# Kernel tuning notes

Measured on AMD Instinct MI355X. Metric: run time of the kernel, lower is better.

The kernel has to match this reference:

```python
import jax, jax.numpy as jnp
import numpy as np

D_MODEL, D_K, D_V, N_HEADS = 1024, 64, 64, 16
BS, N_CTX = 2, 2048


def setup_inputs() -> dict:
    key = jax.random.key(0)
    ks = jax.random.split(key, 8)
    s = 0.02
    return {
        "x": jax.random.normal(ks[0], (BS, N_CTX, D_MODEL), dtype=jnp.float32),
        "Wq": jax.random.normal(ks[1], (D_K * N_HEADS, D_MODEL), dtype=jnp.float32) * s,
        "bq": jnp.zeros((D_K * N_HEADS,), dtype=jnp.float32),
        "Wk": jax.random.normal(ks[2], (D_K * N_HEADS, D_MODEL), dtype=jnp.float32) * s,
        "bk": jnp.zeros((D_K * N_HEADS,), dtype=jnp.float32),
        "Wv": jax.random.normal(ks[3], (D_V * N_HEADS, D_MODEL), dtype=jnp.float32) * s,
        "bv": jnp.zeros((D_V * N_HEADS,), dtype=jnp.float32),
        "Wo": jax.random.normal(ks[4], (D_MODEL, D_V * N_HEADS), dtype=jnp.float32) * s,
    }


def reference(x, Wq, bq, Wk, bk, Wv, bv, Wo):
    bs, n_ctx, d_model = x.shape
    # projections (torch Linear: y = x @ W.T + b)
    q = x @ Wq.T + bq  # (bs, n, H*dk)
    k = x @ Wk.T + bk
    v = x @ Wv.T + bv
    split = lambda t, d: t.reshape(bs, n_ctx, N_HEADS, d).transpose(0, 2, 1, 3)
    Q, K, V = split(q, D_K), split(k, D_K), split(v, D_V)  # (bs, H, n, d)
    scores = jnp.einsum('bhqd,bhkd->bhqk', Q / jnp.sqrt(jnp.float32(D_K)), K)
    # causal mask: x + (1 - 1/tril(ones)) == 0 on/below diag, -inf above
    causal = jnp.tril(jnp.ones((n_ctx, n_ctx), dtype=bool))
    scores = jnp.where(causal, scores, -jnp.inf)
    attn = jax.nn.softmax(scores, axis=-1)
    out = jnp.einsum('bhqk,bhkd->bhqd', attn, V)  # (bs, H, n, dv)
    out = out.transpose(0, 2, 1, 3).reshape(bs, n_ctx, N_HEADS * D_V)
    return out @ Wo.T  # no bias on output projection
```

## Files before the change

kernel.cpp:

```cpp
#include <hip/hip_runtime.h>
#include <hip/hip_bf16.h>


using bf16x8   = __attribute__((ext_vector_type(8))) __bf16;
using f32x4    = __attribute__((ext_vector_type(4))) float;
using ushort4v = __attribute__((ext_vector_type(4))) unsigned short;

__device__ __forceinline__ unsigned short f2bf(float f) {
    unsigned int u = __float_as_uint(f);
    u += 0x7FFFu + ((u >> 16) & 1u);
    return (unsigned short)(u >> 16);
}

__device__ __forceinline__ unsigned cvtpk(float lo, float hi) {
    unsigned r;
    asm("v_cvt_pk_bf16_f32 %0, %1, %2" : "=v"(r) : "v"(lo), "v"(hi));
    return r;
}

__device__ __forceinline__ void gll16(const void* g, void* l) {
    __builtin_amdgcn_global_load_lds(
        (const __attribute__((address_space(1))) void*)g,
        (__attribute__((address_space(3))) void*)l, 16, 0, 0);
}

__global__ __launch_bounds__(256) void cast_bf16_kernel(
    const float* __restrict__ in, unsigned short* __restrict__ out, int n4) {
    int i = blockIdx.x * 256 + threadIdx.x;
    if (i >= n4) return;
    float4 f = reinterpret_cast<const float4*>(in)[i];
    ushort4v o;
    o.x = f2bf(f.x); o.y = f2bf(f.y); o.z = f2bf(f.z); o.w = f2bf(f.w);
    reinterpret_cast<ushort4v*>(out)[i] = o;
}

__global__ __launch_bounds__(256) void cast_w4_kernel(
    const float* __restrict__ w0, const float* __restrict__ w1,
    const float* __restrict__ w2, const float* __restrict__ w3,
    unsigned short* __restrict__ o0, unsigned short* __restrict__ o1,
    unsigned short* __restrict__ o2, unsigned short* __restrict__ o3) {
    const int z = blockIdx.y;
    const float* in = (z == 0) ? w0 : (z == 1) ? w1 : (z == 2) ? w2 : w3;
    unsigned short* out = (z == 0) ? o0 : (z == 1) ? o1 : (z == 2) ? o2 : o3;
    int i = blockIdx.x * 256 + threadIdx.x;
    float4 f = reinterpret_cast<const float4*>(in)[i];
    ushort4v o;
    o.x = f2bf(f.x); o.y = f2bf(f.y); o.z = f2bf(f.z); o.w = f2bf(f.w);
    reinterpret_cast<ushort4v*>(out)[i] = o;
}

__device__ __forceinline__ void gemm_core_128x64(
    const unsigned short* __restrict__ A, const unsigned short* __restrict__ B,
    int m0, int n0, int K,
    unsigned short* As, unsigned short* Bs, f32x4 acc[4][2]) {
    const int tid = threadIdx.x;
    const int lane = tid & 63;
    const int wid = tid >> 6;
    const int wr = wid >> 1, wc = wid & 1;
    const int l16 = lane & 15, lg = lane >> 4;

#pragma unroll
    for (int i = 0; i < 4; i++)
#pragma unroll
        for (int j = 0; j < 2; j++) acc[i][j] = f32x4{0.f, 0.f, 0.f, 0.f};

    const int srow = lane >> 2;
    const int scol = (lane & 3) * 8;
    const unsigned short* Ab0 = &A[(size_t)(m0 + wid * 16 + srow) * K + scol];
    const unsigned short* Ab1 = &A[(size_t)(m0 + 64 + wid * 16 + srow) * K + scol];
    const unsigned short* Bb0 = &B[(size_t)(n0 + wid * 16 + srow) * K + scol];
    unsigned short* AsW0 = As + (wid * 16) * 32;
    unsigned short* AsW1 = As + (64 + wid * 16) * 32;
    unsigned short* BsW0 = Bs + (wid * 16) * 32;

    for (int k0 = 0; k0 < K; k0 += 32) {
        __syncthreads();
        gll16(Ab0 + k0, AsW0);
        gll16(Ab1 + k0, AsW1);
        gll16(Bb0 + k0, BsW0);
        __syncthreads();
        bf16x8 af[4], bfr[2];
#pragma unroll
        for (int i = 0; i < 4; i++)
            af[i] = *reinterpret_cast<const bf16x8*>(&As[(64 * wr + 16 * i + l16) * 32 + 8 * lg]);
#pragma unroll
        for (int j = 0; j < 2; j++)
            bfr[j] = *reinterpret_cast<const bf16x8*>(&Bs[(32 * wc + 16 * j + l16) * 32 + 8 * lg]);
#pragma unroll
        for (int i = 0; i < 4; i++)
#pragma unroll
            for (int j = 0; j < 2; j++)
                acc[i][j] = __builtin_amdgcn_mfma_f32_16x16x32_bf16(af[i], bfr[j], acc[i][j], 0, 0, 0);
    }
}

__global__ __launch_bounds__(256) void gemm_qkv_kernel(
    const unsigned short* __restrict__ xbf,
    const unsigned short* __restrict__ wq, const unsigned short* __restrict__ wk,
    const unsigned short* __restrict__ wv,
    const float* __restrict__ bq, const float* __restrict__ bk, const float* __restrict__ bv,
    unsigned short* __restrict__ q_ws, unsigned short* __restrict__ k_ws,
    unsigned short* __restrict__ vt_ws) {
    __shared__ __align__(16) unsigned short As[128 * 32];
    __shared__ __align__(16) unsigned short Bs[64 * 32];
    const int z = blockIdx.z;
    const unsigned short* W = (z == 0) ? wq : ((z == 1) ? wk : wv);
    const float* bias = (z == 0) ? bq : ((z == 1) ? bk : bv);
    const float scale = (z == 0) ? 0.125f * 1.44269504f : 1.0f;
    const int m0 = blockIdx.y * 128;
    const int n0 = blockIdx.x * 64;

    f32x4 acc[4][2];
    gemm_core_128x64(xbf, W, m0, n0, 1024, As, Bs, acc);

    const int tid = threadIdx.x;
    const int lane = tid & 63;
    const int wid = tid >> 6;
    const int wr = wid >> 1, wc = wid & 1;
    const int l16 = lane & 15, lg = lane >> 4;

#pragma unroll
    for (int j = 0; j < 2; j++) {
        const int c = n0 + 32 * wc + 16 * j + l16;
        const float bc = bias[c];
        const int h = c >> 6, d = c & 63;
#pragma unroll
        for (int i = 0; i < 4; i++) {
            const int mb = m0 + 64 * wr + 16 * i + 4 * lg;
            if (z < 2) {
                unsigned short* dst = (z == 0) ? q_ws : k_ws;
#pragma unroll
                for (int r = 0; r < 4; r++) {
                    int m = mb + r;
                    int b = m >> 11, n = m & 2047;
                    float v = (acc[i][j][r] + bc) * scale;
                    dst[(((b * 16 + h) * 2048 + n) << 6) + d] = f2bf(v);
                }
            } else {
                int b = mb >> 11, n = mb & 2047;
                ushort4v pk;
                pk.x = f2bf(acc[i][j][0] + bc);
                pk.y = f2bf(acc[i][j][1] + bc);
                pk.z = f2bf(acc[i][j][2] + bc);
                pk.w = f2bf(acc[i][j][3] + bc);
                *reinterpret_cast<ushort4v*>(&vt_ws[((b * 16 + h) * 64 + d) * 2048 + n]) = pk;
            }
        }
    }
}

__global__ __launch_bounds__(256) void attn_kernel(
    const unsigned short* __restrict__ q_ws, const unsigned short* __restrict__ k_ws,
    const unsigned short* __restrict__ vt_ws, unsigned short* __restrict__ attn_out) {
    __shared__ __align__(16) unsigned short P_lds[4][2][16][40];
    const int tid = threadIdx.x;
    const int wid = tid >> 6, lane = tid & 63;
    const int l16 = lane & 15, lg = lane >> 4;
    const int gwid = blockIdx.x * 4 + wid;
    const int bh = gwid >> 6;
    const int p = gwid & 63;
    const int qA0 = p << 4;
    const int qB0 = 2032 - (p << 4);
    const unsigned short* qb = q_ws + bh * (2048 * 64);
    const unsigned short* kb = k_ws + bh * (2048 * 64);
    const unsigned short* vb = vt_ws + bh * (64 * 2048);

    bf16x8 aqA0 = *reinterpret_cast<const bf16x8*>(&qb[(qA0 + l16) * 64 + 8 * lg]);
    bf16x8 aqA1 = *reinterpret_cast<const bf16x8*>(&qb[(qA0 + l16) * 64 + 32 + 8 * lg]);
    bf16x8 aqB0 = *reinterpret_cast<const bf16x8*>(&qb[(qB0 + l16) * 64 + 8 * lg]);
    bf16x8 aqB1 = *reinterpret_cast<const bf16x8*>(&qb[(qB0 + l16) * 64 + 32 + 8 * lg]);

    f32x4 oA[4], oB[4];
#pragma unroll
    for (int j = 0; j < 4; j++) { oA[j] = f32x4{0.f, 0.f, 0.f, 0.f}; oB[j] = f32x4{0.f, 0.f, 0.f, 0.f}; }
    float mA = -1e30f, lA = 0.f, mB = -1e30f, lB = 0.f;

    bf16x8 k00 = *reinterpret_cast<const bf16x8*>(&kb[l16 * 64 + 8 * lg]);
    bf16x8 k01 = *reinterpret_cast<const bf16x8*>(&kb[l16 * 64 + 32 + 8 * lg]);
    bf16x8 k10 = *reinterpret_cast<const bf16x8*>(&kb[(16 + l16) * 64 + 8 * lg]);
    bf16x8 k11 = *reinterpret_cast<const bf16x8*>(&kb[(16 + l16) * 64 + 32 + 8 * lg]);

    const int kvEnd = qB0 + 16;
    for (int kv0 = 0; kv0 < kvEnd; kv0 += 32) {
        bf16x8 v0 = *reinterpret_cast<const bf16x8*>(&vb[l16 * 2048 + kv0 + 8 * lg]);
        bf16x8 v1 = *reinterpret_cast<const bf16x8*>(&vb[(16 + l16) * 2048 + kv0 + 8 * lg]);
        bf16x8 v2 = *reinterpret_cast<const bf16x8*>(&vb[(32 + l16) * 2048 + kv0 + 8 * lg]);
        bf16x8 v3 = *reinterpret_cast<const bf16x8*>(&vb[(48 + l16) * 2048 + kv0 + 8 * lg]);

        const f32x4 z = f32x4{0.f, 0.f, 0.f, 0.f};
        f32x4 sB0 = __builtin_amdgcn_mfma_f32_16x16x32_bf16(k00, aqB0, z, 0, 0, 0);
        sB0 = __builtin_amdgcn_mfma_f32_16x16x32_bf16(k01, aqB1, sB0, 0, 0, 0);
        f32x4 sB1 = __builtin_amdgcn_mfma_f32_16x16x32_bf16(k10, aqB0, z, 0, 0, 0);
        sB1 = __builtin_amdgcn_mfma_f32_16x16x32_bf16(k11, aqB1, sB1, 0, 0, 0);
        const bool actA = kv0 < qA0 + 16;
        f32x4 sA0 = z, sA1 = z;
        if (actA) {
            sA0 = __builtin_amdgcn_mfma_f32_16x16x32_bf16(k00, aqA0, z, 0, 0, 0);
            sA0 = __builtin_amdgcn_mfma_f32_16x16x32_bf16(k01, aqA1, sA0, 0, 0, 0);
            sA1 = __builtin_amdgcn_mfma_f32_16x16x32_bf16(k10, aqA0, z, 0, 0, 0);
            sA1 = __builtin_amdgcn_mfma_f32_16x16x32_bf16(k11, aqA1, sA1, 0, 0, 0);
        }
        if (kv0 + 32 < kvEnd) {
            const unsigned short* kr0 = &kb[(kv0 + 32 + l16) * 64 + 8 * lg];
            const unsigned short* kr1 = &kb[(kv0 + 48 + l16) * 64 + 8 * lg];
            k00 = *reinterpret_cast<const bf16x8*>(kr0);
            k01 = *reinterpret_cast<const bf16x8*>(kr0 + 32);
            k10 = *reinterpret_cast<const bf16x8*>(kr1);
            k11 = *reinterpret_cast<const bf16x8*>(kr1 + 32);
        }

        auto process = [&](f32x4 s0, f32x4 s1, int qX0, float& mX, float& lX,
                           f32x4* o, int slot, bool diag) {
            if (diag) {
                const int kbase = kv0 + 4 * lg;
                const int qrow = qX0 + l16;
#pragma unroll
                for (int r = 0; r < 4; r++) {
                    if (kbase + r > qrow) s0[r] = -1e30f;
                    if (kbase + 16 + r > qrow) s1[r] = -1e30f;
                }
            }
            float mx = fmaxf(fmaxf(fmaxf(s0[0], s0[1]), fmaxf(s0[2], s0[3])),
                             fmaxf(fmaxf(s1[0], s1[1]), fmaxf(s1[2], s1[3])));
            mx = fmaxf(mx, __shfl_xor(mx, 16));
            mx = fmaxf(mx, __shfl_xor(mx, 32));
            if (!__all(mx <= mX + 8.0f)) {
                const float mnew = fmaxf(mX, mx);
                const float sf = __builtin_amdgcn_exp2f(mX - mnew);
                mX = mnew;
                lX *= sf;
                float sfT[4];
#pragma unroll
                for (int r = 0; r < 4; r++) sfT[r] = __shfl(sf, 4 * lg + r);
#pragma unroll
                for (int j = 0; j < 4; j++) {
                    o[j][0] *= sfT[0]; o[j][1] *= sfT[1];
                    o[j][2] *= sfT[2]; o[j][3] *= sfT[3];
                }
            }
            float p0[4], p1[4];
#pragma unroll
            for (int r = 0; r < 4; r++) {
                p0[r] = __builtin_amdgcn_exp2f(s0[r] - mX);
                p1[r] = __builtin_amdgcn_exp2f(s1[r] - mX);
            }
            float sum = ((p0[0] + p0[1]) + (p0[2] + p0[3])) +
                        ((p1[0] + p1[1]) + (p1[2] + p1[3]));
            sum += __shfl_xor(sum, 16);
            sum += __shfl_xor(sum, 32);
            lX += sum;
            uint2 w0 = make_uint2(cvtpk(p0[0], p0[1]), cvtpk(p0[2], p0[3]));
            uint2 w1 = make_uint2(cvtpk(p1[0], p1[1]), cvtpk(p1[2], p1[3]));
            *reinterpret_cast<uint2*>(&P_lds[wid][slot][l16][4 * lg]) = w0;
            *reinterpret_cast<uint2*>(&P_lds[wid][slot][l16][16 + 4 * lg]) = w1;
            bf16x8 pf = *reinterpret_cast<const bf16x8*>(&P_lds[wid][slot][l16][8 * lg]);
            o[0] = __builtin_amdgcn_mfma_f32_16x16x32_bf16(pf, v0, o[0], 0, 0, 0);
            o[1] = __builtin_amdgcn_mfma_f32_16x16x32_bf16(pf, v1, o[1], 0, 0, 0);
            o[2] = __builtin_amdgcn_mfma_f32_16x16x32_bf16(pf, v2, o[2], 0, 0, 0);
            o[3] = __builtin_amdgcn_mfma_f32_16x16x32_bf16(pf, v3, o[3], 0, 0, 0);
        };
        const bool diagB = (kv0 + 32 >= kvEnd);
        process(sB0, sB1, qB0, mB, lB, oB, 1, diagB);
        if (actA) {
            const bool diagA = (kv0 + 32 >= qA0 + 16);
            process(sA0, sA1, qA0, mA, lA, oA, 0, diagA);
        }
    }

    const int b = bh >> 4, h = bh & 15;
    auto epi = [&](int qX0, float lX, f32x4* o) {
        float inv[4];
#pragma unroll
        for (int r = 0; r < 4; r++) inv[r] = 1.0f / __shfl(lX, 4 * lg + r);
#pragma unroll
        for (int j = 0; j < 4; j++)
#pragma unroll
            for (int r = 0; r < 4; r++) {
                int n = qX0 + 4 * lg + r;
                attn_out[(size_t)(b * 2048 + n) * 1024 + h * 64 + 16 * j + l16] =
                    f2bf(o[j][r] * inv[r]);
            }
    };
    epi(qA0, lA, oA);
    epi(qB0, lB, oB);
}

__global__ __launch_bounds__(256) void gemm_out_kernel(
    const unsigned short* __restrict__ abf, const unsigned short* __restrict__ wo,
    float* __restrict__ out) {
    __shared__ __align__(16) unsigned short As[128 * 32];
    __shared__ __align__(16) unsigned short Bs[64 * 32];
    const int m0 = blockIdx.y * 128;
    const int n0 = blockIdx.x * 64;
    f32x4 acc[4][2];
    gemm_core_128x64(abf, wo, m0, n0, 1024, As, Bs, acc);

    const int tid = threadIdx.x;
    const int lane = tid & 63;
    const int wid = tid >> 6;
    const int wr = wid >> 1, wc = wid & 1;
    const int l16 = lane & 15, lg = lane >> 4;
#pragma unroll
    for (int j = 0; j < 2; j++) {
        const int c = n0 + 32 * wc + 16 * j + l16;
#pragma unroll
        for (int i = 0; i < 4; i++) {
#pragma unroll
            for (int r = 0; r < 4; r++) {
                int m = m0 + 64 * wr + 16 * i + 4 * lg + r;
                out[(size_t)m * 1024 + c] = acc[i][j][r];
            }
        }
    }
}

extern "C" void kernel_launch(void* const* d_in, const int* in_sizes, int n_in,
                              void* d_out, int out_size, void* d_ws, size_t ws_size,
                              hipStream_t stream) {
    const float* x  = (const float*)d_in[0];
    const float* Wq = (const float*)d_in[1];
    const float* bq = (const float*)d_in[2];
    const float* Wk = (const float*)d_in[3];
    const float* bk = (const float*)d_in[4];
    const float* Wv = (const float*)d_in[5];
    const float* bv = (const float*)d_in[6];
    const float* Wo = (const float*)d_in[7];
    float* out = (float*)d_out;

    char* ws = (char*)d_ws;
    unsigned short* xbf  = (unsigned short*)(ws);
    unsigned short* wqbf = (unsigned short*)(ws + (8u  << 20));
    unsigned short* wkbf = (unsigned short*)(ws + (10u << 20));
    unsigned short* wvbf = (unsigned short*)(ws + (12u << 20));
    unsigned short* wobf = (unsigned short*)(ws + (14u << 20));
    unsigned short* qws  = (unsigned short*)(ws + (16u << 20));
    unsigned short* kws  = (unsigned short*)(ws + (24u << 20));
    unsigned short* vtws = (unsigned short*)(ws + (32u << 20));
    unsigned short* aows = (unsigned short*)(ws + (40u << 20));

    cast_bf16_kernel<<<4096, 256, 0, stream>>>(x, xbf, 4096 * 1024 / 4);
    cast_w4_kernel<<<dim3(1024, 4), 256, 0, stream>>>(
        Wq, Wk, Wv, Wo, wqbf, wkbf, wvbf, wobf);

    gemm_qkv_kernel<<<dim3(16, 32, 3), 256, 0, stream>>>(
        xbf, wqbf, wkbf, wvbf, bq, bk, bv, qws, kws, vtws);

    attn_kernel<<<512, 256, 0, stream>>>(qws, kws, vtws, aows);

    gemm_out_kernel<<<dim3(16, 32), 256, 0, stream>>>(aows, wobf, out);
}
```

Before: 274.1 us.

## Rework attention to one Q tile per wave with XCD mapping and K/V double buffering

The attention kernel no longer pairs a short and a long query tile per wave. Each wave now handles a single 16-row query tile, and blocks are mapped so that heads stay on the same XCD. K and V are prefetched through a two-stage register double buffer, and setprio is raised around the MFMA sections. Separately, the QKV projection GEMM grows its tile to 128x128, which gives more reuse per block. The cost is worse load balance across causal work, since wave lengths now vary with query position, and higher register pressure under the new launch bound.

```diff
diff --git a/kernel.cpp b/kernel.cpp
--- a/kernel.cpp
+++ b/kernel.cpp
@@ -49,6 +49,54 @@
     reinterpret_cast<ushort4v*>(out)[i] = o;
 }
 
+__device__ __forceinline__ void gemm_core_128(
+    const unsigned short* __restrict__ A, const unsigned short* __restrict__ B,
+    int m0, int n0, int K,
+    unsigned short* As, unsigned short* Bs, f32x4 acc[4][4]) {
+    const int tid = threadIdx.x;
+    const int lane = tid & 63;
+    const int wid = tid >> 6;
+    const int wr = wid >> 1, wc = wid & 1;
+    const int l16 = lane & 15, lg = lane >> 4;
+
+#pragma unroll
+    for (int i = 0; i < 4; i++)
+#pragma unroll
+        for (int j = 0; j < 4; j++) acc[i][j] = f32x4{0.f, 0.f, 0.f, 0.f};
+
+    const int srow = lane >> 2;
+    const int scol = (lane & 3) * 8;
+    const unsigned short* Ab0 = &A[(size_t)(m0 + wid * 16 + srow) * K + scol];
+    const unsigned short* Ab1 = &A[(size_t)(m0 + 64 + wid * 16 + srow) * K + scol];
+    const unsigned short* Bb0 = &B[(size_t)(n0 + wid * 16 + srow) * K + scol];
+    const unsigned short* Bb1 = &B[(size_t)(n0 + 64 + wid * 16 + srow) * K + scol];
+    unsigned short* AsW0 = As + (wid * 16) * 32;
+    unsigned short* AsW1 = As + (64 + wid * 16) * 32;
+    unsigned short* BsW0 = Bs + (wid * 16) * 32;
+    unsigned short* BsW1 = Bs + (64 + wid * 16) * 32;
+
+    for (int k0 = 0; k0 < K; k0 += 32) {
+        __syncthreads();
+        gll16(Ab0 + k0, AsW0);
+        gll16(Ab1 + k0, AsW1);
+        gll16(Bb0 + k0, BsW0);
+        gll16(Bb1 + k0, BsW1);
+        __syncthreads();
+        bf16x8 af[4], bfr[4];
+#pragma unroll
+        for (int i = 0; i < 4; i++)
+            af[i] = *reinterpret_cast<const bf16x8*>(&As[(64 * wr + 16 * i + l16) * 32 + 8 * lg]);
+#pragma unroll
+        for (int j = 0; j < 4; j++)
+            bfr[j] = *reinterpret_cast<const bf16x8*>(&Bs[(64 * wc + 16 * j + l16) * 32 + 8 * lg]);
+#pragma unroll
+        for (int i = 0; i < 4; i++)
+#pragma unroll
+            for (int j = 0; j < 4; j++)
+                acc[i][j] = __builtin_amdgcn_mfma_f32_16x16x32_bf16(af[i], bfr[j], acc[i][j], 0, 0, 0);
+    }
+}
+
 __device__ __forceinline__ void gemm_core_128x64(
     const unsigned short* __restrict__ A, const unsigned short* __restrict__ B,
     int m0, int n0, int K,
@@ -102,16 +150,16 @@
     unsigned short* __restrict__ q_ws, unsigned short* __restrict__ k_ws,
     unsigned short* __restrict__ vt_ws) {
     __shared__ __align__(16) unsigned short As[128 * 32];
-    __shared__ __align__(16) unsigned short Bs[64 * 32];
+    __shared__ __align__(16) unsigned short Bs[128 * 32];
     const int z = blockIdx.z;
     const unsigned short* W = (z == 0) ? wq : ((z == 1) ? wk : wv);
     const float* bias = (z == 0) ? bq : ((z == 1) ? bk : bv);
     const float scale = (z == 0) ? 0.125f * 1.44269504f : 1.0f;
     const int m0 = blockIdx.y * 128;
-    const int n0 = blockIdx.x * 64;
-
-    f32x4 acc[4][2];
-    gemm_core_128x64(xbf, W, m0, n0, 1024, As, Bs, acc);
+    const int n0 = blockIdx.x * 128;
+
+    f32x4 acc[4][4];
+    gemm_core_128(xbf, W, m0, n0, 1024, As, Bs, acc);
 
     const int tid = threadIdx.x;
     const int lane = tid & 63;
@@ -120,8 +168,8 @@
     const int l16 = lane & 15, lg = lane >> 4;
 
 #pragma unroll
-    for (int j = 0; j < 2; j++) {
-        const int c = n0 + 32 * wc + 16 * j + l16;
+    for (int j = 0; j < 4; j++) {
+        const int c = n0 + 64 * wc + 16 * j + l16;
         const float bc = bias[c];
         const int h = c >> 6, d = c & 63;
 #pragma unroll
@@ -149,140 +197,151 @@
     }
 }
 
-__global__ __launch_bounds__(256) void attn_kernel(
+__global__ __launch_bounds__(256, 4) void attn_kernel(
     const unsigned short* __restrict__ q_ws, const unsigned short* __restrict__ k_ws,
     const unsigned short* __restrict__ vt_ws, unsigned short* __restrict__ attn_out) {
-    __shared__ __align__(16) unsigned short P_lds[4][2][16][40];
+    __shared__ __align__(16) unsigned short P_lds[4][16][40];
     const int tid = threadIdx.x;
     const int wid = tid >> 6, lane = tid & 63;
     const int l16 = lane & 15, lg = lane >> 4;
-    const int gwid = blockIdx.x * 4 + wid;
-    const int bh = gwid >> 6;
-    const int p = gwid & 63;
-    const int qA0 = p << 4;
-    const int qB0 = 2032 - (p << 4);
+    const int bid = blockIdx.x;
+    const int xcd = bid & 7, idx = bid >> 3;
+    const int bh = xcd * 4 + (idx >> 5);
+    const int t = ((idx & 31) << 2) + wid;
+    const int q0 = t << 4;
     const unsigned short* qb = q_ws + bh * (2048 * 64);
     const unsigned short* kb = k_ws + bh * (2048 * 64);
     const unsigned short* vb = vt_ws + bh * (64 * 2048);
 
-    bf16x8 aqA0 = *reinterpret_cast<const bf16x8*>(&qb[(qA0 + l16) * 64 + 8 * lg]);
-    bf16x8 aqA1 = *reinterpret_cast<const bf16x8*>(&qb[(qA0 + l16) * 64 + 32 + 8 * lg]);
-    bf16x8 aqB0 = *reinterpret_cast<const bf16x8*>(&qb[(qB0 + l16) * 64 + 8 * lg]);
-    bf16x8 aqB1 = *reinterpret_cast<const bf16x8*>(&qb[(qB0 + l16) * 64 + 32 + 8 * lg]);
-
-    f32x4 oA[4], oB[4];
-#pragma unroll
-    for (int j = 0; j < 4; j++) { oA[j] = f32x4{0.f, 0.f, 0.f, 0.f}; oB[j] = f32x4{0.f, 0.f, 0.f, 0.f}; }
-    float mA = -1e30f, lA = 0.f, mB = -1e30f, lB = 0.f;
-
-    bf16x8 k00 = *reinterpret_cast<const bf16x8*>(&kb[l16 * 64 + 8 * lg]);
-    bf16x8 k01 = *reinterpret_cast<const bf16x8*>(&kb[l16 * 64 + 32 + 8 * lg]);
-    bf16x8 k10 = *reinterpret_cast<const bf16x8*>(&kb[(16 + l16) * 64 + 8 * lg]);
-    bf16x8 k11 = *reinterpret_cast<const bf16x8*>(&kb[(16 + l16) * 64 + 32 + 8 * lg]);
-
-    const int kvEnd = qB0 + 16;
-    for (int kv0 = 0; kv0 < kvEnd; kv0 += 32) {
-        bf16x8 v0 = *reinterpret_cast<const bf16x8*>(&vb[l16 * 2048 + kv0 + 8 * lg]);
-        bf16x8 v1 = *reinterpret_cast<const bf16x8*>(&vb[(16 + l16) * 2048 + kv0 + 8 * lg]);
-        bf16x8 v2 = *reinterpret_cast<const bf16x8*>(&vb[(32 + l16) * 2048 + kv0 + 8 * lg]);
-        bf16x8 v3 = *reinterpret_cast<const bf16x8*>(&vb[(48 + l16) * 2048 + kv0 + 8 * lg]);
-
-        const f32x4 z = f32x4{0.f, 0.f, 0.f, 0.f};
-        f32x4 sB0 = __builtin_amdgcn_mfma_f32_16x16x32_bf16(k00, aqB0, z, 0, 0, 0);
-        sB0 = __builtin_amdgcn_mfma_f32_16x16x32_bf16(k01, aqB1, sB0, 0, 0, 0);
-        f32x4 sB1 = __builtin_amdgcn_mfma_f32_16x16x32_bf16(k10, aqB0, z, 0, 0, 0);
-        sB1 = __builtin_amdgcn_mfma_f32_16x16x32_bf16(k11, aqB1, sB1, 0, 0, 0);
-        const bool actA = kv0 < qA0 + 16;
-        f32x4 sA0 = z, sA1 = z;
-        if (actA) {
-            sA0 = __builtin_amdgcn_mfma_f32_16x16x32_bf16(k00, aqA0, z, 0, 0, 0);
-            sA0 = __builtin_amdgcn_mfma_f32_16x16x32_bf16(k01, aqA1, sA0, 0, 0, 0);
-            sA1 = __builtin_amdgcn_mfma_f32_16x16x32_bf16(k10, aqA0, z, 0, 0, 0);
-            sA1 = __builtin_amdgcn_mfma_f32_16x16x32_bf16(k11, aqA1, sA1, 0, 0, 0);
-        }
-        if (kv0 + 32 < kvEnd) {
-            const unsigned short* kr0 = &kb[(kv0 + 32 + l16) * 64 + 8 * lg];
-            const unsigned short* kr1 = &kb[(kv0 + 48 + l16) * 64 + 8 * lg];
-            k00 = *reinterpret_cast<const bf16x8*>(kr0);
-            k01 = *reinterpret_cast<const bf16x8*>(kr0 + 32);
-            k10 = *reinterpret_cast<const bf16x8*>(kr1);
-            k11 = *reinterpret_cast<const bf16x8*>(kr1 + 32);
-        }
-
-        auto process = [&](f32x4 s0, f32x4 s1, int qX0, float& mX, float& lX,
-                           f32x4* o, int slot, bool diag) {
-            if (diag) {
-                const int kbase = kv0 + 4 * lg;
-                const int qrow = qX0 + l16;
-#pragma unroll
-                for (int r = 0; r < 4; r++) {
-                    if (kbase + r > qrow) s0[r] = -1e30f;
-                    if (kbase + 16 + r > qrow) s1[r] = -1e30f;
-                }
+    bf16x8 aq0 = *reinterpret_cast<const bf16x8*>(&qb[(q0 + l16) * 64 + 8 * lg]);
+    bf16x8 aq1 = *reinterpret_cast<const bf16x8*>(&qb[(q0 + l16) * 64 + 32 + 8 * lg]);
+
+    f32x4 o[4];
+#pragma unroll
+    for (int j = 0; j < 4; j++) o[j] = f32x4{0.f, 0.f, 0.f, 0.f};
+    float mX = -1e30f, lX = 0.f;
+
+    const int kvEnd = q0 + 16;
+
+    auto process = [&](const bf16x8& c00, const bf16x8& c01,
+                       const bf16x8& c10, const bf16x8& c11,
+                       const bf16x8& w0, const bf16x8& w1,
+                       const bf16x8& w2, const bf16x8& w3,
+                       int kv0, bool diag) {
+        const f32x4 zz = f32x4{0.f, 0.f, 0.f, 0.f};
+        __builtin_amdgcn_s_setprio(1);
+        f32x4 s0 = __builtin_amdgcn_mfma_f32_16x16x32_bf16(c00, aq0, zz, 0, 0, 0);
+        s0 = __builtin_amdgcn_mfma_f32_16x16x32_bf16(c01, aq1, s0, 0, 0, 0);
+        f32x4 s1 = __builtin_amdgcn_mfma_f32_16x16x32_bf16(c10, aq0, zz, 0, 0, 0);
+        s1 = __builtin_amdgcn_mfma_f32_16x16x32_bf16(c11, aq1, s1, 0, 0, 0);
+        __builtin_amdgcn_s_setprio(0);
+        if (diag) {
+            const int kbase = kv0 + 4 * lg;
+            const int qrow = q0 + l16;
+#pragma unroll
+            for (int r = 0; r < 4; r++) {
+                if (kbase + r > qrow) s0[r] = -1e30f;
+                if (kbase + 16 + r > qrow) s1[r] = -1e30f;
             }
-            float mx = fmaxf(fmaxf(fmaxf(s0[0], s0[1]), fmaxf(s0[2], s0[3])),
-                             fmaxf(fmaxf(s1[0], s1[1]), fmaxf(s1[2], s1[3])));
-            mx = fmaxf(mx, __shfl_xor(mx, 16));
-            mx = fmaxf(mx, __shfl_xor(mx, 32));
-            if (!__all(mx <= mX + 8.0f)) {
-                const float mnew = fmaxf(mX, mx);
-                const float sf = __builtin_amdgcn_exp2f(mX - mnew);
-                mX = mnew;
-                lX *= sf;
-                float sfT[4];
-#pragma unroll
-                for (int r = 0; r < 4; r++) sfT[r] = __shfl(sf, 4 * lg + r);
-#pragma unroll
-                for (int j = 0; j < 4; j++) {
-                    o[j][0] *= sfT[0]; o[j][1] *= sfT[1];
-                    o[j][2] *= sfT[2]; o[j][3] *= sfT[3];
-                }
+        }
+        float mx = fmaxf(fmaxf(fmaxf(s0[0], s0[1]), fmaxf(s0[2], s0[3])),
+                         fmaxf(fmaxf(s1[0], s1[1]), fmaxf(s1[2], s1[3])));
+        mx = fmaxf(mx, __shfl_xor(mx, 16));
+        mx = fmaxf(mx, __shfl_xor(mx, 32));
+        if (!__all(mx <= mX + 8.0f)) {
+            const float mnew = fmaxf(mX, mx);
+            const float sf = __builtin_amdgcn_exp2f(mX - mnew);
+            mX = mnew;
+            lX *= sf;
+            float sfT[4];
+#pragma unroll
+            for (int r = 0; r < 4; r++) sfT[r] = __shfl(sf, 4 * lg + r);
+#pragma unroll
+            for (int j = 0; j < 4; j++) {
+                o[j][0] *= sfT[0]; o[j][1] *= sfT[1];
+                o[j][2] *= sfT[2]; o[j][3] *= sfT[3];
             }
-            float p0[4], p1[4];
-#pragma unroll
-            for (int r = 0; r < 4; r++) {
-                p0[r] = __builtin_amdgcn_exp2f(s0[r] - mX);
-                p1[r] = __builtin_amdgcn_exp2f(s1[r] - mX);
-            }
-            float sum = ((p0[0] + p0[1]) + (p0[2] + p0[3])) +
-                        ((p1[0] + p1[1]) + (p1[2] + p1[3]));
-            sum += __shfl_xor(sum, 16);
-            sum += __shfl_xor(sum, 32);
-            lX += sum;
-            uint2 w0 = make_uint2(cvtpk(p0[0], p0[1]), cvtpk(p0[2], p0[3]));
-            uint2 w1 = make_uint2(cvtpk(p1[0], p1[1]), cvtpk(p1[2], p1[3]));
-            *reinterpret_cast<uint2*>(&P_lds[wid][slot][l16][4 * lg]) = w0;
-            *reinterpret_cast<uint2*>(&P_lds[wid][slot][l16][16 + 4 * lg]) = w1;
-            bf16x8 pf = *reinterpret_cast<const bf16x8*>(&P_lds[wid][slot][l16][8 * lg]);
-            o[0] = __builtin_amdgcn_mfma_f32_16x16x32_bf16(pf, v0, o[0], 0, 0, 0);
-            o[1] = __builtin_amdgcn_mfma_f32_16x16x32_bf16(pf, v1, o[1], 0, 0, 0);
-            o[2] = __builtin_amdgcn_mfma_f32_16x16x32_bf16(pf, v2, o[2], 0, 0, 0);
-            o[3] = __builtin_amdgcn_mfma_f32_16x16x32_bf16(pf, v3, o[3], 0, 0, 0);
-        };
-        const bool diagB = (kv0 + 32 >= kvEnd);
-        process(sB0, sB1, qB0, mB, lB, oB, 1, diagB);
-        if (actA) {
-            const bool diagA = (kv0 + 32 >= qA0 + 16);
-            process(sA0, sA1, qA0, mA, lA, oA, 0, diagA);
-        }
+        }
+        float p0[4], p1[4];
+#pragma unroll
+        for (int r = 0; r < 4; r++) {
+            p0[r] = __builtin_amdgcn_exp2f(s0[r] - mX);
+            p1[r] = __builtin_amdgcn_exp2f(s1[r] - mX);
+        }
+        float sum = ((p0[0] + p0[1]) + (p0[2] + p0[3])) +
+                    ((p1[0] + p1[1]) + (p1[2] + p1[3]));
+        sum += __shfl_xor(sum, 16);
+        sum += __shfl_xor(sum, 32);
+        lX += sum;
+        uint2 w0p = make_uint2(cvtpk(p0[0], p0[1]), cvtpk(p0[2], p0[3]));
+        uint2 w1p = make_uint2(cvtpk(p1[0], p1[1]), cvtpk(p1[2], p1[3]));
+        *reinterpret_cast<uint2*>(&P_lds[wid][l16][4 * lg]) = w0p;
+        *reinterpret_cast<uint2*>(&P_lds[wid][l16][16 + 4 * lg]) = w1p;
+        bf16x8 pf = *reinterpret_cast<const bf16x8*>(&P_lds[wid][l16][8 * lg]);
+        __builtin_amdgcn_s_setprio(1);
+        o[0] = __builtin_amdgcn_mfma_f32_16x16x32_bf16(pf, w0, o[0], 0, 0, 0);
+        o[1] = __builtin_amdgcn_mfma_f32_16x16x32_bf16(pf, w1, o[1], 0, 0, 0);
+        o[2] = __builtin_amdgcn_mfma_f32_16x16x32_bf16(pf, w2, o[2], 0, 0, 0);
+        o[3] = __builtin_amdgcn_mfma_f32_16x16x32_bf16(pf, w3, o[3], 0, 0, 0);
+        __builtin_amdgcn_s_setprio(0);
+    };
+
+    bf16x8 kA0 = *reinterpret_cast<const bf16x8*>(&kb[l16 * 64 + 8 * lg]);
+    bf16x8 kA1 = *reinterpret_cast<const bf16x8*>(&kb[l16 * 64 + 32 + 8 * lg]);
+    bf16x8 kA2 = *reinterpret_cast<const bf16x8*>(&kb[(16 + l16) * 64 + 8 * lg]);
+    bf16x8 kA3 = *reinterpret_cast<const bf16x8*>(&kb[(16 + l16) * 64 + 32 + 8 * lg]);
+    bf16x8 vA0 = *reinterpret_cast<const bf16x8*>(&vb[l16 * 2048 + 8 * lg]);
+    bf16x8 vA1 = *reinterpret_cast<const bf16x8*>(&vb[(16 + l16) * 2048 + 8 * lg]);
+    bf16x8 vA2 = *reinterpret_cast<const bf16x8*>(&vb[(32 + l16) * 2048 + 8 * lg]);
+    bf16x8 vA3 = *reinterpret_cast<const bf16x8*>(&vb[(48 + l16) * 2048 + 8 * lg]);
+
+    int kv0 = 0;
+    for (;;) {
+        bool last = (kv0 + 32 >= kvEnd);
+        bf16x8 kB0, kB1, kB2, kB3, vB0, vB1, vB2, vB3;
+        if (!last) {
+            const int kn = kv0 + 32;
+            kB0 = *reinterpret_cast<const bf16x8*>(&kb[(kn + l16) * 64 + 8 * lg]);
+            kB1 = *reinterpret_cast<const bf16x8*>(&kb[(kn + l16) * 64 + 32 + 8 * lg]);
+            kB2 = *reinterpret_cast<const bf16x8*>(&kb[(kn + 16 + l16) * 64 + 8 * lg]);
+            kB3 = *reinterpret_cast<const bf16x8*>(&kb[(kn + 16 + l16) * 64 + 32 + 8 * lg]);
+            vB0 = *reinterpret_cast<const bf16x8*>(&vb[l16 * 2048 + kn + 8 * lg]);
+            vB1 = *reinterpret_cast<const bf16x8*>(&vb[(16 + l16) * 2048 + kn + 8 * lg]);
+            vB2 = *reinterpret_cast<const bf16x8*>(&vb[(32 + l16) * 2048 + kn + 8 * lg]);
+            vB3 = *reinterpret_cast<const bf16x8*>(&vb[(48 + l16) * 2048 + kn + 8 * lg]);
+        }
+        process(kA0, kA1, kA2, kA3, vA0, vA1, vA2, vA3, kv0, last);
+        kv0 += 32;
+        if (last) break;
+        last = (kv0 + 32 >= kvEnd);
+        if (!last) {
+            const int kn = kv0 + 32;
+            kA0 = *reinterpret_cast<const bf16x8*>(&kb[(kn + l16) * 64 + 8 * lg]);
+            kA1 = *reinterpret_cast<const bf16x8*>(&kb[(kn + l16) * 64 + 32 + 8 * lg]);
+            kA2 = *reinterpret_cast<const bf16x8*>(&kb[(kn + 16 + l16) * 64 + 8 * lg]);
+            kA3 = *reinterpret_cast<const bf16x8*>(&kb[(kn + 16 + l16) * 64 + 32 + 8 * lg]);
+            vA0 = *reinterpret_cast<const bf16x8*>(&vb[l16 * 2048 + kn + 8 * lg]);
+            vA1 = *reinterpret_cast<const bf16x8*>(&vb[(16 + l16) * 2048 + kn + 8 * lg]);
+            vA2 = *reinterpret_cast<const bf16x8*>(&vb[(32 + l16) * 2048 + kn + 8 * lg]);
+            vA3 = *reinterpret_cast<const bf16x8*>(&vb[(48 + l16) * 2048 + kn + 8 * lg]);
+        }
+        process(kB0, kB1, kB2, kB3, vB0, vB1, vB2, vB3, kv0, last);
+        kv0 += 32;
+        if (last) break;
     }
 
     const int b = bh >> 4, h = bh & 15;
-    auto epi = [&](int qX0, float lX, f32x4* o) {
-        float inv[4];
-#pragma unroll
-        for (int r = 0; r < 4; r++) inv[r] = 1.0f / __shfl(lX, 4 * lg + r);
-#pragma unroll
-        for (int j = 0; j < 4; j++)
-#pragma unroll
-            for (int r = 0; r < 4; r++) {
-                int n = qX0 + 4 * lg + r;
-                attn_out[(size_t)(b * 2048 + n) * 1024 + h * 64 + 16 * j + l16] =
-                    f2bf(o[j][r] * inv[r]);
-            }
-    };
-    epi(qA0, lA, oA);
-    epi(qB0, lB, oB);
+    float inv[4];
+#pragma unroll
+    for (int r = 0; r < 4; r++) inv[r] = 1.0f / __shfl(lX, 4 * lg + r);
+#pragma unroll
+    for (int j = 0; j < 4; j++)
+#pragma unroll
+        for (int r = 0; r < 4; r++) {
+            int n = q0 + 4 * lg + r;
+            attn_out[(size_t)(b * 2048 + n) * 1024 + h * 64 + 16 * j + l16] =
+                f2bf(o[j][r] * inv[r]);
+        }
 }
 
 __global__ __launch_bounds__(256) void gemm_out_kernel(
@@ -342,10 +401,10 @@
     cast_w4_kernel<<<dim3(1024, 4), 256, 0, stream>>>(
         Wq, Wk, Wv, Wo, wqbf, wkbf, wvbf, wobf);
 
-    gemm_qkv_kernel<<<dim3(16, 32, 3), 256, 0, stream>>>(
+    gemm_qkv_kernel<<<dim3(8, 32, 3), 256, 0, stream>>>(
         xbf, wqbf, wkbf, wvbf, bq, bk, bv, qws, kws, vtws);
 
-    attn_kernel<<<512, 256, 0, stream>>>(qws, kws, vtws, aows);
+    attn_kernel<<<1024, 256, 0, stream>>>(qws, kws, vtws, aows);
 
     gemm_out_kernel<<<dim3(16, 32), 256, 0, stream>>>(aows, wobf, out);
 }
```

After: 401.1 us. 46.3% more time.

## Enlarge QKV GEMM tile to 128x128 and remap attention blocks per XCD

Applied to the files above, without the earlier changes.

The QKV projection GEMM now uses a 128x128 output tile with a 4x4 MFMA accumulator per wave instead of 128x64. This halves the grid in N and raises arithmetic intensity per LDS load. The attention kernel's block-to-(batch-head, query-pair) mapping is also permuted so that blocks landing on the same XCD (bid & 7) share the same heads, aiming for better L2 reuse of K/V. The costs are higher register pressure from 64 accumulator floats and fewer blocks in the QKV GEMM (768).

```diff
diff --git a/kernel.cpp b/kernel.cpp
--- a/kernel.cpp
+++ b/kernel.cpp
@@ -49,6 +49,54 @@
     reinterpret_cast<ushort4v*>(out)[i] = o;
 }
 
+__device__ __forceinline__ void gemm_core_128(
+    const unsigned short* __restrict__ A, const unsigned short* __restrict__ B,
+    int m0, int n0, int K,
+    unsigned short* As, unsigned short* Bs, f32x4 acc[4][4]) {
+    const int tid = threadIdx.x;
+    const int lane = tid & 63;
+    const int wid = tid >> 6;
+    const int wr = wid >> 1, wc = wid & 1;
+    const int l16 = lane & 15, lg = lane >> 4;
+
+#pragma unroll
+    for (int i = 0; i < 4; i++)
+#pragma unroll
+        for (int j = 0; j < 4; j++) acc[i][j] = f32x4{0.f, 0.f, 0.f, 0.f};
+
+    const int srow = lane >> 2;
+    const int scol = (lane & 3) * 8;
+    const unsigned short* Ab0 = &A[(size_t)(m0 + wid * 16 + srow) * K + scol];
+    const unsigned short* Ab1 = &A[(size_t)(m0 + 64 + wid * 16 + srow) * K + scol];
+    const unsigned short* Bb0 = &B[(size_t)(n0 + wid * 16 + srow) * K + scol];
+    const unsigned short* Bb1 = &B[(size_t)(n0 + 64 + wid * 16 + srow) * K + scol];
+    unsigned short* AsW0 = As + (wid * 16) * 32;
+    unsigned short* AsW1 = As + (64 + wid * 16) * 32;
+    unsigned short* BsW0 = Bs + (wid * 16) * 32;
+    unsigned short* BsW1 = Bs + (64 + wid * 16) * 32;
+
+    for (int k0 = 0; k0 < K; k0 += 32) {
+        __syncthreads();
+        gll16(Ab0 + k0, AsW0);
+        gll16(Ab1 + k0, AsW1);
+        gll16(Bb0 + k0, BsW0);
+        gll16(Bb1 + k0, BsW1);
+        __syncthreads();
+        bf16x8 af[4], bfr[4];
+#pragma unroll
+        for (int i = 0; i < 4; i++)
+            af[i] = *reinterpret_cast<const bf16x8*>(&As[(64 * wr + 16 * i + l16) * 32 + 8 * lg]);
+#pragma unroll
+        for (int j = 0; j < 4; j++)
+            bfr[j] = *reinterpret_cast<const bf16x8*>(&Bs[(64 * wc + 16 * j + l16) * 32 + 8 * lg]);
+#pragma unroll
+        for (int i = 0; i < 4; i++)
+#pragma unroll
+            for (int j = 0; j < 4; j++)
+                acc[i][j] = __builtin_amdgcn_mfma_f32_16x16x32_bf16(af[i], bfr[j], acc[i][j], 0, 0, 0);
+    }
+}
+
 __device__ __forceinline__ void gemm_core_128x64(
     const unsigned short* __restrict__ A, const unsigned short* __restrict__ B,
     int m0, int n0, int K,
@@ -102,16 +150,16 @@
     unsigned short* __restrict__ q_ws, unsigned short* __restrict__ k_ws,
     unsigned short* __restrict__ vt_ws) {
     __shared__ __align__(16) unsigned short As[128 * 32];
-    __shared__ __align__(16) unsigned short Bs[64 * 32];
+    __shared__ __align__(16) unsigned short Bs[128 * 32];
     const int z = blockIdx.z;
     const unsigned short* W = (z == 0) ? wq : ((z == 1) ? wk : wv);
     const float* bias = (z == 0) ? bq : ((z == 1) ? bk : bv);
     const float scale = (z == 0) ? 0.125f * 1.44269504f : 1.0f;
     const int m0 = blockIdx.y * 128;
-    const int n0 = blockIdx.x * 64;
-
-    f32x4 acc[4][2];
-    gemm_core_128x64(xbf, W, m0, n0, 1024, As, Bs, acc);
+    const int n0 = blockIdx.x * 128;
+
+    f32x4 acc[4][4];
+    gemm_core_128(xbf, W, m0, n0, 1024, As, Bs, acc);
 
     const int tid = threadIdx.x;
     const int lane = tid & 63;
@@ -120,8 +168,8 @@
     const int l16 = lane & 15, lg = lane >> 4;
 
 #pragma unroll
-    for (int j = 0; j < 2; j++) {
-        const int c = n0 + 32 * wc + 16 * j + l16;
+    for (int j = 0; j < 4; j++) {
+        const int c = n0 + 64 * wc + 16 * j + l16;
         const float bc = bias[c];
         const int h = c >> 6, d = c & 63;
 #pragma unroll
@@ -156,9 +204,10 @@
     const int tid = threadIdx.x;
     const int wid = tid >> 6, lane = tid & 63;
     const int l16 = lane & 15, lg = lane >> 4;
-    const int gwid = blockIdx.x * 4 + wid;
-    const int bh = gwid >> 6;
-    const int p = gwid & 63;
+    const int bid = blockIdx.x;
+    const int xcd = bid & 7, idx = bid >> 3;
+    const int bh = xcd * 4 + (idx >> 4);
+    const int p = ((idx & 15) << 2) + wid;
     const int qA0 = p << 4;
     const int qB0 = 2032 - (p << 4);
     const unsigned short* qb = q_ws + bh * (2048 * 64);
@@ -342,7 +391,7 @@
     cast_w4_kernel<<<dim3(1024, 4), 256, 0, stream>>>(
         Wq, Wk, Wv, Wo, wqbf, wkbf, wvbf, wobf);
 
-    gemm_qkv_kernel<<<dim3(16, 32, 3), 256, 0, stream>>>(
+    gemm_qkv_kernel<<<dim3(8, 32, 3), 256, 0, stream>>>(
         xbf, wqbf, wkbf, wvbf, bq, bk, bv, qws, kws, vtws);
 
     attn_kernel<<<512, 256, 0, stream>>>(qws, kws, vtws, aows);
```

Measured after the change: 276.7 us. Within noise of the previous version (+1.0%).
